# Kernel optimization log

Measured on AMD Instinct MI355X. Metric: run time of the kernel, lower is better.

The kernel has to match this reference:

```python
import jax, jax.numpy as jnp
import numpy as np

LEVEL = 8
THRESHOLD = 0.1
INV_SQRT2 = 0.7071067811865476  # 1/sqrt(2), db1 (Haar) filter coefficient

# Static frequency-order permutation: pywt get_level(order='freq') places the
# natural-order (path-lex: aa,ad,da,dd,...) node n at frequency position gray(n).
_g = np.arange(2 ** LEVEL)
_FREQ_PERM = np.argsort(_g ^ (_g >> 1))  # freq[j] = natural[_FREQ_PERM[j]]


def setup_inputs() -> dict:
    key = jax.random.key(0)
    x = jax.random.normal(key, (128, 65536), dtype=jnp.float32)
    return {"x": x}


def _wavelet_packet_leaves(x):
    """Full db1 wavelet-packet tree to LEVEL; returns [B, 2^L, T/2^L] in freq order.

    For Haar with even-length inputs, pywt's symmetric extension is a no-op:
    a[k] = (x[2k]+x[2k+1])/sqrt2, d[k] = (x[2k]-x[2k+1])/sqrt2.
    """
    B, T = x.shape
    c = x[:, None, :]  # [B, nodes=1, len=T]
    for _ in range(LEVEL):
        ev = c[..., 0::2]
        od = c[..., 1::2]
        a = (ev + od) * INV_SQRT2
        d = (ev - od) * INV_SQRT2
        # interleave children (a,d) adjacent -> natural (path-lex) node order
        c = jnp.concatenate([a[:, :, None, :], d[:, :, None, :]], axis=2)
        c = c.reshape(B, -1, a.shape[-1])
    return c[:, _FREQ_PERM, :]


def reference(x):
    coeffs = _wavelet_packet_leaves(x)          # [B, 2^L, n]
    p = coeffs * coeffs
    p = p / (jnp.sum(p, axis=-1, keepdims=True) + 1e-8)
    entropy = -jnp.sum(p * jnp.log(p + 1e-8), axis=-1)  # [B, 2^L]
    keep = entropy > THRESHOLD                           # [B, 2^L] bool
    # Original returns per-batch stacks of kept nodes (variable length);
    # jit-friendly equivalent: zero out pruned nodes and return the mask.
    out = jnp.where(keep[..., None], coeffs, jnp.zeros((), coeffs.dtype))
    return out, entropy, keep
```

## Files before the change

kernel.cpp:

```cpp
#include <hip/hip_runtime.h>

static constexpr int BROWS = 128;
static constexpr int T     = 65536;
static constexpr int CL    = 256;
static constexpr int NCH   = 256;
static constexpr int NODES = 256;
static constexpr int KG    = 32;
static constexpr int LSTR  = 257;

typedef float nfloat4 __attribute__((ext_vector_type(4)));

__device__ __forceinline__ int freq_pos(int h) {
    unsigned r = __brev((unsigned)h) >> 24;
    return (int)(r ^ (r >> 1));
}

__global__ __launch_bounds__(256) void wht_kernel(const float* __restrict__ x,
                                                  float* __restrict__ coeffs,
                                                  float* __restrict__ part) {
    __shared__ float lds[KG][LSTR];

    const int b    = blockIdx.x >> 3;
    const int kg   = blockIdx.x & 7;
    const int k0   = kg * KG;
    const int lane = threadIdx.x & 63;
    const int wave = threadIdx.x >> 6;

    const float* xb = x + (size_t)b * T;

    int npos[4];
    #pragma unroll
    for (int i = 0; i < 4; ++i) npos[i] = freq_pos(4 * lane + i);
    float regA[4] = {0.f, 0.f, 0.f, 0.f};
    float regB[4] = {0.f, 0.f, 0.f, 0.f};

    #pragma unroll
    for (int c = 0; c < KG / 4; ++c) {
        const int kl = wave * (KG / 4) + c;
        float4 v = *(const float4*)(xb + (size_t)(k0 + kl) * CL + lane * 4);

        float4 w;
        w.x = v.x + v.y; w.y = v.x - v.y;
        w.z = v.z + v.w; w.w = v.z - v.w;
        v.x = w.x + w.z; v.z = w.x - w.z;
        v.y = w.y + w.w; v.w = w.y - w.w;

        #pragma unroll
        for (int s = 0; s < 6; ++s) {
            const int mask = 1 << s;
            float4 o;
            o.x = __shfl_xor(v.x, mask, 64);
            o.y = __shfl_xor(v.y, mask, 64);
            o.z = __shfl_xor(v.z, mask, 64);
            o.w = __shfl_xor(v.w, mask, 64);
            const float sgn = 1.0f - 2.0f * (float)((lane >> s) & 1);
            v.x = fmaf(sgn, v.x, o.x);
            v.y = fmaf(sgn, v.y, o.y);
            v.z = fmaf(sgn, v.z, o.z);
            v.w = fmaf(sgn, v.w, o.w);
        }

        float cv[4] = {v.x * 0.0625f, v.y * 0.0625f, v.z * 0.0625f, v.w * 0.0625f};
        #pragma unroll
        for (int i = 0; i < 4; ++i) {
            const float s2 = cv[i] * cv[i];
            regA[i] += s2;
            regB[i] += s2 * __logf(s2 + 1e-35f);
            lds[kl][npos[i]] = cv[i];
        }
    }
    __syncthreads();

    float* ob = coeffs + (size_t)b * T + k0;
    const int kk = (threadIdx.x & 7) * 4;
    const int m0 = threadIdx.x >> 3;
    #pragma unroll
    for (int p = 0; p < 8; ++p) {
        const int m = p * 32 + m0;
        nfloat4 v;
        v.x = lds[kk + 0][m];
        v.y = lds[kk + 1][m];
        v.z = lds[kk + 2][m];
        v.w = lds[kk + 3][m];
        __builtin_nontemporal_store(v, (nfloat4*)(ob + (size_t)m * NCH + kk));
    }
    __syncthreads();

    float* pl = &lds[0][0];
    #pragma unroll
    for (int i = 0; i < 4; ++i) {
        pl[wave * 512 + npos[i]]       = regA[i];
        pl[wave * 512 + 256 + npos[i]] = regB[i];
    }
    __syncthreads();

    const int n = threadIdx.x;
    const float A = pl[n] + pl[512 + n] + pl[1024 + n] + pl[1536 + n];
    const float B = pl[256 + n] + pl[768 + n] + pl[1280 + n] + pl[1792 + n];
    float* pp = part + (size_t)blockIdx.x * 512;
    pp[n]       = A;
    pp[256 + n] = B;
}

__global__ __launch_bounds__(256) void finalize_kernel(const float* __restrict__ part,
                                                       float* __restrict__ coeffs,
                                                       float* __restrict__ entropy,
                                                       float* __restrict__ keep) {
    const int row = blockIdx.x * 256 + threadIdx.x;
    const int b = row >> 8;
    const int n = row & 255;

    float A = 0.f, B = 0.f;
    #pragma unroll
    for (int g = 0; g < 8; ++g) {
        const float* p = part + (size_t)(b * 8 + g) * 512;
        A += p[n];
        B += p[256 + n];
    }

    const float S = A + 1e-8f;
    const float e = (A * __logf(S) - B) / S;
    const bool kp = e > 0.1f;

    entropy[row] = e;
    keep[row]    = kp ? 1.0f : 0.0f;

    if (!kp) {
        float4 z = make_float4(0.f, 0.f, 0.f, 0.f);
        float4* cp = (float4*)(coeffs + (size_t)row * NCH);
        #pragma unroll
        for (int j = 0; j < NCH / 4; ++j) cp[j] = z;
    }
}

extern "C" void kernel_launch(void* const* d_in, const int* in_sizes, int n_in,
                              void* d_out, int out_size, void* d_ws, size_t ws_size,
                              hipStream_t stream) {
    const float* x = (const float*)d_in[0];

    float* coeffs  = (float*)d_out;
    float* entropy = coeffs + (size_t)BROWS * NODES * NCH;
    float* keepf   = entropy + (size_t)BROWS * NODES;

    float* part = (float*)d_ws;

    wht_kernel<<<dim3(BROWS * (NCH / KG)), dim3(256), 0, stream>>>(x, coeffs, part);
    finalize_kernel<<<dim3(BROWS * NODES / 256), dim3(256), 0, stream>>>(part, coeffs, entropy, keepf);
}
```

Baseline: 88.41 us.

## Split Haar transform across half-waves with in-register top butterfly stage

Each half-wave now processes one 256-sample chunk, with each lane holding 8 values. Combining element i with element i+128 handles the top butterfly stage in registers, which drops one of the six cross-lane shuffle stages. That means five shuffle stages over eight values instead of six over four, and it doubles the chunks in flight per load. Partial sums are then merged across the two halves with a shuffle before the LDS reduction. The nontemporal coefficient stores are also replaced with plain stores, which may change cache behaviour for the large output write.

```diff
diff --git a/kernel.cpp b/kernel.cpp
--- a/kernel.cpp
+++ b/kernel.cpp
@@ -8,11 +8,17 @@
 static constexpr int KG    = 32;
 static constexpr int LSTR  = 257;
 
-typedef float nfloat4 __attribute__((ext_vector_type(4)));
-
 __device__ __forceinline__ int freq_pos(int h) {
     unsigned r = __brev((unsigned)h) >> 24;
     return (int)(r ^ (r >> 1));
+}
+
+__device__ __forceinline__ void bfly01(float4& v) {
+    float4 w;
+    w.x = v.x + v.y; w.y = v.x - v.y;
+    w.z = v.z + v.w; w.w = v.z - v.w;
+    v.x = w.x + w.z; v.z = w.x - w.z;
+    v.y = w.y + w.w; v.w = w.y - w.w;
 }
 
 __global__ __launch_bounds__(256) void wht_kernel(const float* __restrict__ x,
@@ -25,48 +31,62 @@
     const int k0   = kg * KG;
     const int lane = threadIdx.x & 63;
     const int wave = threadIdx.x >> 6;
+    const int half = lane >> 5;
+    const int L    = lane & 31;
 
     const float* xb = x + (size_t)b * T;
 
-    int npos[4];
+    int npos1[4], npos2[4];
     #pragma unroll
-    for (int i = 0; i < 4; ++i) npos[i] = freq_pos(4 * lane + i);
-    float regA[4] = {0.f, 0.f, 0.f, 0.f};
-    float regB[4] = {0.f, 0.f, 0.f, 0.f};
+    for (int i = 0; i < 4; ++i) {
+        npos1[i] = freq_pos(4 * L + i);
+        npos2[i] = freq_pos(128 + 4 * L + i);
+    }
+    float A1[4] = {0.f,0.f,0.f,0.f}, B1[4] = {0.f,0.f,0.f,0.f};
+    float A2[4] = {0.f,0.f,0.f,0.f}, B2[4] = {0.f,0.f,0.f,0.f};
 
     #pragma unroll
-    for (int c = 0; c < KG / 4; ++c) {
-        const int kl = wave * (KG / 4) + c;
-        float4 v = *(const float4*)(xb + (size_t)(k0 + kl) * CL + lane * 4);
+    for (int it = 0; it < 4; ++it) {
+        const int kl = wave * 8 + it * 2 + half;
+        const float* cp = xb + (size_t)(k0 + kl) * CL + 4 * L;
+        float4 v1 = *(const float4*)(cp);
+        float4 v2 = *(const float4*)(cp + 128);
 
-        float4 w;
-        w.x = v.x + v.y; w.y = v.x - v.y;
-        w.z = v.z + v.w; w.w = v.z - v.w;
-        v.x = w.x + w.z; v.z = w.x - w.z;
-        v.y = w.y + w.w; v.w = w.y - w.w;
+        float4 t;
+        t.x = v1.x - v2.x; t.y = v1.y - v2.y; t.z = v1.z - v2.z; t.w = v1.w - v2.w;
+        v1.x += v2.x; v1.y += v2.y; v1.z += v2.z; v1.w += v2.w;
+        v2 = t;
+
+        bfly01(v1);
+        bfly01(v2);
 
         #pragma unroll
-        for (int s = 0; s < 6; ++s) {
+        for (int s = 0; s < 5; ++s) {
             const int mask = 1 << s;
-            float4 o;
-            o.x = __shfl_xor(v.x, mask, 64);
-            o.y = __shfl_xor(v.y, mask, 64);
-            o.z = __shfl_xor(v.z, mask, 64);
-            o.w = __shfl_xor(v.w, mask, 64);
-            const float sgn = 1.0f - 2.0f * (float)((lane >> s) & 1);
-            v.x = fmaf(sgn, v.x, o.x);
-            v.y = fmaf(sgn, v.y, o.y);
-            v.z = fmaf(sgn, v.z, o.z);
-            v.w = fmaf(sgn, v.w, o.w);
+            const float sgn = 1.0f - 2.0f * (float)((L >> s) & 1);
+            float o;
+            o = __shfl_xor(v1.x, mask, 64); v1.x = fmaf(sgn, v1.x, o);
+            o = __shfl_xor(v1.y, mask, 64); v1.y = fmaf(sgn, v1.y, o);
+            o = __shfl_xor(v1.z, mask, 64); v1.z = fmaf(sgn, v1.z, o);
+            o = __shfl_xor(v1.w, mask, 64); v1.w = fmaf(sgn, v1.w, o);
+            o = __shfl_xor(v2.x, mask, 64); v2.x = fmaf(sgn, v2.x, o);
+            o = __shfl_xor(v2.y, mask, 64); v2.y = fmaf(sgn, v2.y, o);
+            o = __shfl_xor(v2.z, mask, 64); v2.z = fmaf(sgn, v2.z, o);
+            o = __shfl_xor(v2.w, mask, 64); v2.w = fmaf(sgn, v2.w, o);
         }
 
-        float cv[4] = {v.x * 0.0625f, v.y * 0.0625f, v.z * 0.0625f, v.w * 0.0625f};
+        float c1[4] = {v1.x*0.0625f, v1.y*0.0625f, v1.z*0.0625f, v1.w*0.0625f};
+        float c2[4] = {v2.x*0.0625f, v2.y*0.0625f, v2.z*0.0625f, v2.w*0.0625f};
         #pragma unroll
         for (int i = 0; i < 4; ++i) {
-            const float s2 = cv[i] * cv[i];
-            regA[i] += s2;
-            regB[i] += s2 * __logf(s2 + 1e-35f);
-            lds[kl][npos[i]] = cv[i];
+            const float s1 = c1[i] * c1[i];
+            A1[i] += s1;
+            B1[i] += s1 * __logf(s1 + 1e-35f);
+            lds[kl][npos1[i]] = c1[i];
+            const float s2 = c2[i] * c2[i];
+            A2[i] += s2;
+            B2[i] += s2 * __logf(s2 + 1e-35f);
+            lds[kl][npos2[i]] = c2[i];
         }
     }
     __syncthreads();
@@ -77,20 +97,29 @@
     #pragma unroll
     for (int p = 0; p < 8; ++p) {
         const int m = p * 32 + m0;
-        nfloat4 v;
+        float4 v;
         v.x = lds[kk + 0][m];
         v.y = lds[kk + 1][m];
         v.z = lds[kk + 2][m];
         v.w = lds[kk + 3][m];
-        __builtin_nontemporal_store(v, (nfloat4*)(ob + (size_t)m * NCH + kk));
+        *(float4*)(ob + (size_t)m * NCH + kk) = v;
     }
     __syncthreads();
 
-    float* pl = &lds[0][0];
     #pragma unroll
     for (int i = 0; i < 4; ++i) {
-        pl[wave * 512 + npos[i]]       = regA[i];
-        pl[wave * 512 + 256 + npos[i]] = regB[i];
+        A1[i] += __shfl_xor(A1[i], 32, 64); B1[i] += __shfl_xor(B1[i], 32, 64);
+        A2[i] += __shfl_xor(A2[i], 32, 64); B2[i] += __shfl_xor(B2[i], 32, 64);
+    }
+    float* pl = &lds[0][0];
+    if (half == 0) {
+        #pragma unroll
+        for (int i = 0; i < 4; ++i) {
+            pl[wave * 512 + npos1[i]]       = A1[i];
+            pl[wave * 512 + 256 + npos1[i]] = B1[i];
+            pl[wave * 512 + npos2[i]]       = A2[i];
+            pl[wave * 512 + 256 + npos2[i]] = B2[i];
+        }
     }
     __syncthreads();
 
```

After: 87.20 us. About the same (-1.4%).

## Restructure WHT lane mapping to use in-register and DPP butterflies, fuse entropy partials

Applied to the files above, without the earlier changes.

Each lane now loads four float4 chunks of a 256-sample chunk and performs two butterfly stages in registers, with 16 lanes per chunk. The cross-lane stages use DPP quad and row permutes instead of ds_bpermute shuffles, leaving only one shuffle stage. Entropy partial sums are computed during the transposed store loop, reduced with DPP and shuffles, and written directly, which removes two barriers and the LDS reduction. Nontemporal stores become plain stores, which may change how the coefficient writes interact with the cache.

```diff
diff --git a/kernel.cpp b/kernel.cpp
--- a/kernel.cpp
+++ b/kernel.cpp
@@ -8,11 +8,47 @@
 static constexpr int KG    = 32;
 static constexpr int LSTR  = 257;
 
-typedef float nfloat4 __attribute__((ext_vector_type(4)));
-
 __device__ __forceinline__ int freq_pos(int h) {
     unsigned r = __brev((unsigned)h) >> 24;
     return (int)(r ^ (r >> 1));
+}
+
+__device__ __forceinline__ void bflyreg(float4& u, float4& v) {
+    float4 t;
+    t.x = u.x - v.x; t.y = u.y - v.y; t.z = u.z - v.z; t.w = u.w - v.w;
+    u.x += v.x; u.y += v.y; u.z += v.z; u.w += v.w;
+    v = t;
+}
+
+__device__ __forceinline__ void bfly01(float4& v) {
+    float4 w;
+    w.x = v.x + v.y; w.y = v.x - v.y;
+    w.z = v.z + v.w; w.w = v.z - v.w;
+    v.x = w.x + w.z; v.z = w.x - w.z;
+    v.y = w.y + w.w; v.w = w.y - w.w;
+}
+
+template<int CTRL>
+__device__ __forceinline__ float xchg_dpp(float v) {
+    return __builtin_bit_cast(float,
+        __builtin_amdgcn_update_dpp(0, __builtin_bit_cast(int, v), CTRL, 0xF, 0xF, true));
+}
+
+template<int CTRL>
+__device__ __forceinline__ void stage_dpp1(float4& v, float sgn) {
+    float o;
+    o = xchg_dpp<CTRL>(v.x); v.x = fmaf(sgn, v.x, o);
+    o = xchg_dpp<CTRL>(v.y); v.y = fmaf(sgn, v.y, o);
+    o = xchg_dpp<CTRL>(v.z); v.z = fmaf(sgn, v.z, o);
+    o = xchg_dpp<CTRL>(v.w); v.w = fmaf(sgn, v.w, o);
+}
+
+__device__ __forceinline__ void stage_shfl1(float4& v, float sgn, int mask) {
+    float o;
+    o = __shfl_xor(v.x, mask, 64); v.x = fmaf(sgn, v.x, o);
+    o = __shfl_xor(v.y, mask, 64); v.y = fmaf(sgn, v.y, o);
+    o = __shfl_xor(v.z, mask, 64); v.z = fmaf(sgn, v.z, o);
+    o = __shfl_xor(v.w, mask, 64); v.w = fmaf(sgn, v.w, o);
 }
 
 __global__ __launch_bounds__(256) void wht_kernel(const float* __restrict__ x,
@@ -23,83 +59,88 @@
     const int b    = blockIdx.x >> 3;
     const int kg   = blockIdx.x & 7;
     const int k0   = kg * KG;
-    const int lane = threadIdx.x & 63;
-    const int wave = threadIdx.x >> 6;
+    const int tid  = threadIdx.x;
+    const int lane = tid & 63;
+    const int wave = tid >> 6;
+    const int p    = lane & 15;
+    const int cg   = lane >> 4;
 
     const float* xb = x + (size_t)b * T;
 
-    int npos[4];
+    const int p0 = p & 1, p1 = (p >> 1) & 1, p2 = (p >> 2) & 1, p3 = (p >> 3) & 1;
+    const int offs = 4 * p0 + 8 * p1 + 32 * p2 + 64 * p3;
+
+    int npos[4][4];
     #pragma unroll
-    for (int i = 0; i < 4; ++i) npos[i] = freq_pos(4 * lane + i);
-    float regA[4] = {0.f, 0.f, 0.f, 0.f};
-    float regB[4] = {0.f, 0.f, 0.f, 0.f};
+    for (int q = 0; q < 4; ++q)
+        #pragma unroll
+        for (int i = 0; i < 4; ++i)
+            npos[q][i] = freq_pos(i + offs + 16 * (q & 1) + 128 * (q >> 1));
+
+    const float sA = 1.0f - 2.0f * (float)p0;
+    const float sB = 1.0f - 2.0f * (float)p1;
+    const float sC = 1.0f - 2.0f * (float)p2;
+    const float sD = 1.0f - 2.0f * (float)p3;
 
     #pragma unroll
-    for (int c = 0; c < KG / 4; ++c) {
-        const int kl = wave * (KG / 4) + c;
-        float4 v = *(const float4*)(xb + (size_t)(k0 + kl) * CL + lane * 4);
+    for (int it = 0; it < 2; ++it) {
+        const int kl = wave * 8 + it * 4 + cg;
+        const float* cp = xb + (size_t)(k0 + kl) * CL + offs;
+        float4 V0 = *(const float4*)(cp);
+        float4 V1 = *(const float4*)(cp + 16);
+        float4 V2 = *(const float4*)(cp + 128);
+        float4 V3 = *(const float4*)(cp + 144);
 
-        float4 w;
-        w.x = v.x + v.y; w.y = v.x - v.y;
-        w.z = v.z + v.w; w.w = v.z - v.w;
-        v.x = w.x + w.z; v.z = w.x - w.z;
-        v.y = w.y + w.w; v.w = w.y - w.w;
+        bflyreg(V0, V2); bflyreg(V1, V3);
+        bflyreg(V0, V1); bflyreg(V2, V3);
+        bfly01(V0); bfly01(V1); bfly01(V2); bfly01(V3);
+        stage_dpp1<0xB1>(V0, sA); stage_dpp1<0xB1>(V1, sA);
+        stage_dpp1<0xB1>(V2, sA); stage_dpp1<0xB1>(V3, sA);
+        stage_dpp1<0x4E>(V0, sB); stage_dpp1<0x4E>(V1, sB);
+        stage_dpp1<0x4E>(V2, sB); stage_dpp1<0x4E>(V3, sB);
+        stage_shfl1(V0, sC, 4);   stage_shfl1(V1, sC, 4);
+        stage_shfl1(V2, sC, 4);   stage_shfl1(V3, sC, 4);
+        stage_dpp1<0x128>(V0, sD); stage_dpp1<0x128>(V1, sD);
+        stage_dpp1<0x128>(V2, sD); stage_dpp1<0x128>(V3, sD);
 
-        #pragma unroll
-        for (int s = 0; s < 6; ++s) {
-            const int mask = 1 << s;
-            float4 o;
-            o.x = __shfl_xor(v.x, mask, 64);
-            o.y = __shfl_xor(v.y, mask, 64);
-            o.z = __shfl_xor(v.z, mask, 64);
-            o.w = __shfl_xor(v.w, mask, 64);
-            const float sgn = 1.0f - 2.0f * (float)((lane >> s) & 1);
-            v.x = fmaf(sgn, v.x, o.x);
-            v.y = fmaf(sgn, v.y, o.y);
-            v.z = fmaf(sgn, v.z, o.z);
-            v.w = fmaf(sgn, v.w, o.w);
-        }
-
-        float cv[4] = {v.x * 0.0625f, v.y * 0.0625f, v.z * 0.0625f, v.w * 0.0625f};
-        #pragma unroll
-        for (int i = 0; i < 4; ++i) {
-            const float s2 = cv[i] * cv[i];
-            regA[i] += s2;
-            regB[i] += s2 * __logf(s2 + 1e-35f);
-            lds[kl][npos[i]] = cv[i];
-        }
+        float* row = lds[kl];
+        row[npos[0][0]] = V0.x * 0.0625f; row[npos[0][1]] = V0.y * 0.0625f;
+        row[npos[0][2]] = V0.z * 0.0625f; row[npos[0][3]] = V0.w * 0.0625f;
+        row[npos[1][0]] = V1.x * 0.0625f; row[npos[1][1]] = V1.y * 0.0625f;
+        row[npos[1][2]] = V1.z * 0.0625f; row[npos[1][3]] = V1.w * 0.0625f;
+        row[npos[2][0]] = V2.x * 0.0625f; row[npos[2][1]] = V2.y * 0.0625f;
+        row[npos[2][2]] = V2.z * 0.0625f; row[npos[2][3]] = V2.w * 0.0625f;
+        row[npos[3][0]] = V3.x * 0.0625f; row[npos[3][1]] = V3.y * 0.0625f;
+        row[npos[3][2]] = V3.z * 0.0625f; row[npos[3][3]] = V3.w * 0.0625f;
     }
     __syncthreads();
 
     float* ob = coeffs + (size_t)b * T + k0;
-    const int kk = (threadIdx.x & 7) * 4;
-    const int m0 = threadIdx.x >> 3;
+    float* pp = part + (size_t)blockIdx.x * 512;
+    const int kk = (tid & 7) * 4;
+    const int m0 = tid >> 3;
     #pragma unroll
-    for (int p = 0; p < 8; ++p) {
-        const int m = p * 32 + m0;
-        nfloat4 v;
+    for (int pw = 0; pw < 8; ++pw) {
+        const int m = pw * 32 + m0;
+        float4 v;
         v.x = lds[kk + 0][m];
         v.y = lds[kk + 1][m];
         v.z = lds[kk + 2][m];
         v.w = lds[kk + 3][m];
-        __builtin_nontemporal_store(v, (nfloat4*)(ob + (size_t)m * NCH + kk));
+        *(float4*)(ob + (size_t)m * NCH + kk) = v;
+
+        const float qx = v.x * v.x, qy = v.y * v.y, qz = v.z * v.z, qw = v.w * v.w;
+        float A = qx + qy + qz + qw;
+        float B = qx * __logf(qx + 1e-35f) + qy * __logf(qy + 1e-35f)
+                + qz * __logf(qz + 1e-35f) + qw * __logf(qw + 1e-35f);
+        A += xchg_dpp<0xB1>(A);  B += xchg_dpp<0xB1>(B);
+        A += xchg_dpp<0x4E>(A);  B += xchg_dpp<0x4E>(B);
+        A += __shfl_xor(A, 4, 64); B += __shfl_xor(B, 4, 64);
+        if ((tid & 7) == 0) {
+            pp[m]       = A;
+            pp[256 + m] = B;
+        }
     }
-    __syncthreads();
-
-    float* pl = &lds[0][0];
-    #pragma unroll
-    for (int i = 0; i < 4; ++i) {
-        pl[wave * 512 + npos[i]]       = regA[i];
-        pl[wave * 512 + 256 + npos[i]] = regB[i];
-    }
-    __syncthreads();
-
-    const int n = threadIdx.x;
-    const float A = pl[n] + pl[512 + n] + pl[1024 + n] + pl[1536 + n];
-    const float B = pl[256 + n] + pl[768 + n] + pl[1280 + n] + pl[1792 + n];
-    float* pp = part + (size_t)blockIdx.x * 512;
-    pp[n]       = A;
-    pp[256 + n] = B;
 }
 
 __global__ __launch_bounds__(256) void finalize_kernel(const float* __restrict__ part,
```

New measurement: 86.32 us. -2.4%, faster.
